# Kernel tuning notes

Measured on AMD Instinct MI355X. Metric: run time of the kernel, lower is better.

The kernel has to match this reference:

```python
import jax, jax.numpy as jnp
import numpy as np

EPS = 1e-5
MAX_NORM = 1.0 - 1e-5  # clamp for atanh / ball projection


def mob_add(u, v):
    # Mobius addition on each d_ball (last dim), c=1
    uv = jnp.sum(u * v, axis=-1, keepdims=True)
    uu = jnp.sum(u * u, axis=-1, keepdims=True)
    vv = jnp.sum(v * v, axis=-1, keepdims=True)
    num = (1.0 + 2.0 * uv + vv) * u + (1.0 - uu) * v
    den = 1.0 + 2.0 * uv + uu * vv
    return num / jnp.maximum(den, EPS)


def log_map_zero(y):
    # log map at origin, per ball (last dim)
    n = jnp.linalg.norm(y, axis=-1, keepdims=True)
    n_c = jnp.clip(n, EPS, MAX_NORM)
    return jnp.arctanh(n_c) * y / n_c


def mob_mat_mul_d(W, x, d):
    # W: (n_in, d, n_out, d); x: (B, n_in, d) -> (B, n_out, d)
    # Mobius matvec on the flattened product-ball representation.
    B = x.shape[0]
    x_f = x.reshape(B, -1)                      # (B, n_in*d)
    W_f = W.reshape(x_f.shape[-1], -1)          # (n_in*d, n_out*d)
    Mx = x_f @ W_f                              # (B, n_out*d)
    x_n = jnp.clip(jnp.linalg.norm(x_f, axis=-1, keepdims=True), EPS, MAX_NORM)
    Mx_n = jnp.maximum(jnp.linalg.norm(Mx, axis=-1, keepdims=True), EPS)
    res = jnp.tanh(Mx_n / x_n * jnp.arctanh(x_n)) * (Mx / Mx_n)
    return res.reshape(B, -1, d)


def mob_pointwise_prod(x, u):
    # diagonal Mobius scaling of hyperbolic x by euclidean gate u, per ball
    ux = u * x
    x_n = jnp.clip(jnp.linalg.norm(x, axis=-1, keepdims=True), EPS, MAX_NORM)
    ux_n = jnp.maximum(jnp.linalg.norm(ux, axis=-1, keepdims=True), EPS)
    return jnp.tanh(ux_n / x_n * jnp.arctanh(x_n)) * (ux / ux_n)


def transition(W, h, U, x, b, d):
    Wh = mob_mat_mul_d(W, h, d)
    Ux = mob_mat_mul_d(U, x, d)
    return mob_add(mob_add(Wh, Ux), b)


def setup_inputs() -> dict:
    key = jax.random.key(0)
    ks = jax.random.split(key, 8)
    B, I, H, D = 16384, 256, 256, 4
    k = (1.0 / H) ** 0.5
    # scale points to lie strictly inside the Poincare ball
    hyp_x = 0.02 * jax.random.normal(ks[0], (B, I, D), dtype=jnp.float32)
    hidden = 0.02 * jax.random.normal(ks[1], (B, H, D), dtype=jnp.float32)
    mk = lambda kk, n_in: jax.random.uniform(kk, (n_in, D, H, D), minval=-k, maxval=k, dtype=jnp.float32)
    return dict(
        hyp_x=hyp_x, hidden=hidden,
        w_z=mk(ks[2], H), w_r=mk(ks[3], H), w_h=mk(ks[4], H),
        u_z=mk(ks[5], I), u_r=mk(ks[6], I), u_h=mk(ks[7], I),
        b_z=jnp.zeros((H, D), jnp.float32),
        b_r=jnp.zeros((H, D), jnp.float32),
        b_h=jnp.zeros((H, D), jnp.float32),
    )


def reference(hyp_x, hidden, w_z, w_r, w_h, u_z, u_r, u_h, b_z, b_r, b_h):
    d = hyp_x.shape[-1]
    z = jax.nn.sigmoid(log_map_zero(transition(w_z, hidden, u_z, hyp_x, b_z, d)))
    r = jax.nn.sigmoid(log_map_zero(transition(w_r, hidden, u_r, hyp_x, b_r, d)))
    r_point_h = mob_pointwise_prod(hidden, r)
    # NOTE: original code uses u_r here (not u_h) -- kept faithful
    h_tilde = transition(w_h, r_point_h, u_r, hyp_x, b_h, d)
    minus_h_oplus_htilde = mob_add(-hidden, h_tilde)
    new_h = mob_add(hidden, mob_pointwise_prod(minus_h_oplus_htilde, z))
    return new_h
```

## Files before the change

kernel.cpp:

```cpp
#include <hip/hip_runtime.h>
#include <stdint.h>

#define EPSF 1e-5f
#define MAXNF (1.0f - 1e-5f)

typedef __attribute__((ext_vector_type(8))) short short8;
typedef __attribute__((ext_vector_type(4))) float floatx4;

__device__ __forceinline__ unsigned short f2bf(float f){
  union { float f; uint32_t u; } v; v.f = f;
  return (unsigned short)((v.u + 0x7FFFu + ((v.u >> 16) & 1u)) >> 16);
}
__device__ __forceinline__ float bf_lo(uint32_t u){
  union { uint32_t u; float f; } v; v.u = u << 16; return v.f;
}
__device__ __forceinline__ float bf_hi(uint32_t u){
  union { uint32_t u; float f; } v; v.u = u & 0xffff0000u; return v.f;
}
__device__ __forceinline__ uint32_t cvtpk(float lo, float hi){
  uint32_t r; asm("v_cvt_pk_bf16_f32 %0, %1, %2" : "=v"(r) : "v"(lo), "v"(hi));
  return r;
}
__device__ __forceinline__ float fsqrt(float x){ return __builtin_amdgcn_sqrtf(x); }

__device__ __forceinline__ float4 ld_ball(const unsigned short* rowp, int b){
  const uint2 u = *(const uint2*)(rowp + 4*b);
  return make_float4(bf_lo(u.x), bf_hi(u.x), bf_lo(u.y), bf_hi(u.y));
}
__device__ __forceinline__ void st_ball(unsigned short* rowp, int b, float4 f){
  uint2 u; u.x = cvtpk(f.x, f.y); u.y = cvtpk(f.z, f.w);
  *(uint2*)(rowp + 4*b) = u;
}

__device__ __forceinline__ void gload16(const void* g, void* l){
  __builtin_amdgcn_global_load_lds(
      (__attribute__((address_space(1))) void*)(uintptr_t)g,
      (__attribute__((address_space(3))) void*)l, 16, 0, 0);
}

__device__ __forceinline__ float fatanh(float x){
  return 0.5f * __logf(__fdividef(1.f + x, 1.f - x));
}
__device__ __forceinline__ float ftanh_pos(float x){
  const float t = __expf(-2.f * x);
  return __fdividef(1.f - t, 1.f + t);
}
__device__ __forceinline__ float fsig(float x){
  return __fdividef(1.f, 1.f + __expf(-x));
}

__device__ __forceinline__ float wsum(float v){
  #pragma unroll
  for (int o = 32; o; o >>= 1) v += __shfl_xor(v, o);
  return v;
}

__device__ __forceinline__ float dot4(const float4 a, const float4 b){
  return a.x*b.x + a.y*b.y + a.z*b.z + a.w*b.w;
}
__device__ __forceinline__ float4 scal4(const float4 a, float s){
  return make_float4(a.x*s, a.y*s, a.z*s, a.w*s);
}
__device__ __forceinline__ float clipn(float n){ return fminf(fmaxf(n, EPSF), MAXNF); }

__device__ __forceinline__ float4 mob_add4(const float4 u, const float4 v){
  const float uv = dot4(u,v), uu = dot4(u,u), vv = dot4(v,v);
  const float cu = 1.f + 2.f*uv + vv, cv = 1.f - uu;
  const float inv = __fdividef(1.f, fmaxf(1.f + 2.f*uv + uu*vv, EPSF));
  return make_float4((cu*u.x + cv*v.x)*inv, (cu*u.y + cv*v.y)*inv,
                     (cu*u.z + cv*v.z)*inv, (cu*u.w + cv*v.w)*inv);
}
__device__ __forceinline__ float4 logmap_sig4(const float4 y){
  const float nc = clipn(fsqrt(dot4(y,y)));
  const float s = __fdividef(fatanh(nc), nc);
  return make_float4(fsig(s*y.x), fsig(s*y.y), fsig(s*y.z), fsig(s*y.w));
}
__device__ __forceinline__ float4 mob_pp4(const float4 x, const float4 u){
  const float4 ux = make_float4(u.x*x.x, u.y*x.y, u.z*x.z, u.w*x.w);
  const float xn = clipn(fsqrt(dot4(x,x)));
  const float uxn = fmaxf(fsqrt(dot4(ux,ux)), EPSF);
  const float s = __fdividef(ftanh_pos(__fdividef(uxn, xn) * fatanh(xn)), uxn);
  return scal4(ux, s);
}

__global__ void cast_norm_k(const float* __restrict__ X, unsigned short* __restrict__ Xbf,
                            float* __restrict__ nrm){
  const int lane = threadIdx.x & 63;
  const int row  = blockIdx.x*4 + (threadIdx.x >> 6);
  const float4* xr = (const float4*)(X + (size_t)row*1024);
  unsigned short* br_ = Xbf + (size_t)row*1024;
  float ss = 0.f;
  #pragma unroll
  for (int i = 0; i < 4; ++i){
    const int b = lane + 64*i;
    const float4 v = xr[b];
    st_ball(br_, b, v);
    ss += dot4(v, v);
  }
  ss = wsum(ss);
  if (lane == 0) nrm[row] = fsqrt(ss);
}

__global__ void wcast_k(const float* __restrict__ W, unsigned short* __restrict__ Wt){
  __shared__ float tile[32][33];
  const int tx = threadIdx.x, ty = threadIdx.y;
  const int k0 = blockIdx.x * 32, n0 = blockIdx.y * 32;
  #pragma unroll
  for (int i = 0; i < 4; ++i)
    tile[ty + i*8][tx] = W[(size_t)(k0 + ty + i*8) * 1024 + n0 + tx];
  __syncthreads();
  #pragma unroll
  for (int i = 0; i < 4; ++i)
    Wt[(size_t)(n0 + ty + i*8) * 1024 + k0 + tx] = f2bf(tile[tx][ty + i*8]);
}

#define GBM 128
#define GBN 256
#define GBK 32
#define GKD 1024

__global__ __launch_bounds__(512) void gemm_k(const unsigned short* __restrict__ A,
                                              const unsigned short* __restrict__ Bt,
                                              unsigned short* __restrict__ C,
                                              int lda, int ldc, int lnx){
  __shared__ unsigned short smem[2*4096 + 2*8192];
  unsigned short* As = smem;
  unsigned short* Bs = smem + 2*4096;
  const int tid = threadIdx.x;
  const int lane = tid & 63, w = tid >> 6;
  const int wr = w >> 2, wc = w & 3;
  const int lr = lane & 15, kg = lane >> 4;
  const int wg  = blockIdx.x;
  const int xcd = wg & 7, q = wg >> 3;
  const int bx  = q & ((1 << lnx) - 1);
  const int by  = (xcd << 4) + (q >> lnx);
  const int row0 = by * GBM, col0 = bx * GBN;

  int aoff[4], boff[4];
  #pragma unroll
  for (int a = 0; a < 4; ++a){
    const int r = wr*64 + a*16 + lr;
    aoff[a] = r*32 + ((kg ^ ((r >> 1) & 3)) << 3);
  }
  #pragma unroll
  for (int b = 0; b < 4; ++b){
    const int r = wc*64 + b*16 + lr;
    boff[b] = r*32 + ((kg ^ ((r >> 1) & 3)) << 3);
  }

  floatx4 acc[4][4] = {};

  auto stage = [&](int buf, int kt){
    {
      const int flat = tid;
      const int r = flat >> 2, cp = flat & 3, c = cp ^ ((r >> 1) & 3);
      gload16(A + (size_t)(row0 + r)*lda + kt*GBK + c*8, As + buf*4096 + flat*8);
    }
    #pragma unroll
    for (int i = 0; i < 2; ++i){
      const int flat = i*512 + tid;
      const int r = flat >> 2, cp = flat & 3, c = cp ^ ((r >> 1) & 3);
      gload16(Bt + (size_t)(col0 + r)*GKD + kt*GBK + c*8, Bs + buf*8192 + flat*8);
    }
  };

  stage(0, 0);
  __syncthreads();
  int cur = 0;
  for (int kt = 0; kt < GKD/GBK; ++kt){
    if (kt + 1 < GKD/GBK) stage(cur ^ 1, kt + 1);
    const unsigned short* as = As + cur*4096;
    const unsigned short* bs = Bs + cur*8192;
    short8 af[4], bfv[4];
    #pragma unroll
    for (int a = 0; a < 4; ++a) af[a] = *(const short8*)(as + aoff[a]);
    #pragma unroll
    for (int b = 0; b < 4; ++b) bfv[b] = *(const short8*)(bs + boff[b]);
    #pragma unroll
    for (int a = 0; a < 4; ++a)
      #pragma unroll
      for (int b = 0; b < 4; ++b)
        acc[a][b] = __builtin_amdgcn_mfma_f32_16x16x32_bf16(af[a], bfv[b], acc[a][b], 0, 0, 0);
    __syncthreads();
    cur ^= 1;
  }

  const int crow0 = row0 + wr*64;
  const int ccol = col0 + wc*64 + lr;
  #pragma unroll
  for (int a = 0; a < 4; ++a){
    #pragma unroll
    for (int j = 0; j < 4; ++j){
      const int r = crow0 + a*16 + kg*4 + j;
      unsigned short* cp = C + (size_t)r*ldc + ccol;
      #pragma unroll
      for (int b = 0; b < 4; ++b) cp[b*16] = f2bf(acc[a][b][j]);
    }
  }
}

__global__ __launch_bounds__(256) __attribute__((amdgpu_waves_per_eu(4,4)))
void epi1_k(unsigned short* C1, unsigned short* C2, const unsigned short* hbf,
            const float* bz, const float* br,
            const float* h_nrm, const float* x_nrm, float* rph_nrm){
  const int lane = threadIdx.x & 63;
  const int row  = blockIdx.x*4 + (threadIdx.x >> 6);
  unsigned short* c1lo = C1 + (size_t)row*2048;
  unsigned short* c1hi = c1lo + 1024;
  unsigned short* c2lo = C2 + (size_t)row*2048;
  unsigned short* c2hi = c2lo + 1024;
  const unsigned short* hr = hbf + (size_t)row*1024;

  float4 mzh[4], mrh[4], mzx[4], mrx[4];
  float s0 = 0.f, s1 = 0.f, s2 = 0.f, s3 = 0.f;
  #pragma unroll
  for (int i = 0; i < 4; ++i){
    const int b = lane + 64*i;
    mzh[i] = ld_ball(c1lo, b); mrh[i] = ld_ball(c1hi, b);
    mzx[i] = ld_ball(c2lo, b); mrx[i] = ld_ball(c2hi, b);
    s0 += dot4(mzh[i], mzh[i]); s1 += dot4(mzx[i], mzx[i]);
    s2 += dot4(mrh[i], mrh[i]); s3 += dot4(mrx[i], mrx[i]);
  }
  s0 = wsum(s0); s1 = wsum(s1); s2 = wsum(s2); s3 = wsum(s3);

  const float nMzh = fmaxf(fsqrt(s0), EPSF);
  const float nMzx = fmaxf(fsqrt(s1), EPSF);
  const float nMrh = fmaxf(fsqrt(s2), EPSF);
  const float nMrx = fmaxf(fsqrt(s3), EPSF);
  const float hnc = clipn(h_nrm[row]), xnc = clipn(x_nrm[row]);
  const float atH = fatanh(hnc), atX = fatanh(xnc);
  const float swz = __fdividef(ftanh_pos(__fdividef(nMzh, hnc)*atH), nMzh);
  const float suz = __fdividef(ftanh_pos(__fdividef(nMzx, xnc)*atX), nMzx);
  const float swr = __fdividef(ftanh_pos(__fdividef(nMrh, hnc)*atH), nMrh);
  const float sur = __fdividef(ftanh_pos(__fdividef(nMrx, xnc)*atX), nMrx);

  float sr = 0.f;
  #pragma unroll
  for (int i = 0; i < 4; ++i){
    const int b = lane + 64*i;
    const float4 bz4 = ((const float4*)bz)[b];
    const float4 br4 = ((const float4*)br)[b];
    const float4 z4  = logmap_sig4(mob_add4(mob_add4(scal4(mzh[i],swz), scal4(mzx[i],suz)), bz4));
    const float4 UxR = scal4(mrx[i], sur);
    const float4 r4  = logmap_sig4(mob_add4(mob_add4(scal4(mrh[i],swr), UxR), br4));
    st_ball(c1lo, b, z4);
    st_ball(c1hi, b, UxR);
    const float4 h4  = ld_ball(hr, b);
    const float4 rph = mob_pp4(h4, r4);
    st_ball(c2lo, b, rph);
    sr += dot4(rph, rph);
  }
  sr = wsum(sr);
  if (lane == 0) rph_nrm[row] = fsqrt(sr);
}

__global__ __launch_bounds__(256) __attribute__((amdgpu_waves_per_eu(4,4)))
void epi2_k(const unsigned short* C1, const unsigned short* C2,
            const unsigned short* hbf, const float* bh,
            const float* rph_nrm, float* out){
  const int lane = threadIdx.x & 63;
  const int row  = blockIdx.x*4 + (threadIdx.x >> 6);
  const unsigned short* c1lo = C1 + (size_t)row*2048;
  const unsigned short* c1hi = c1lo + 1024;
  const unsigned short* c2hi = C2 + (size_t)row*2048 + 1024;
  const unsigned short* hr = hbf + (size_t)row*1024;
  float4* outr = (float4*)(out + (size_t)row*1024);

  float4 mh[4];
  float ss = 0.f;
  #pragma unroll
  for (int i = 0; i < 4; ++i){
    mh[i] = ld_ball(c2hi, lane + 64*i);
    ss += dot4(mh[i], mh[i]);
  }
  ss = wsum(ss);
  const float nMh = fmaxf(fsqrt(ss), EPSF);
  const float rnc = clipn(rph_nrm[row]);
  const float swh = __fdividef(ftanh_pos(__fdividef(nMh, rnc)*fatanh(rnc)), nMh);

  #pragma unroll
  for (int i = 0; i < 4; ++i){
    const int b = lane + 64*i;
    const float4 WhH = scal4(mh[i], swh);
    const float4 Ux4 = ld_ball(c1hi, b);
    const float4 bh4 = ((const float4*)bh)[b];
    const float4 ht  = mob_add4(mob_add4(WhH, Ux4), bh4);
    const float4 h4  = ld_ball(hr, b);
    const float4 nh4 = make_float4(-h4.x, -h4.y, -h4.z, -h4.w);
    const float4 m4  = mob_add4(nh4, ht);
    const float4 z4  = ld_ball(c1lo, b);
    const float4 p4  = mob_pp4(m4, z4);
    outr[b] = mob_add4(h4, p4);
  }
}

extern "C" void kernel_launch(void* const* d_in, const int* in_sizes, int n_in,
                              void* d_out, int out_size, void* d_ws, size_t ws_size,
                              hipStream_t stream) {
  (void)in_sizes; (void)n_in; (void)out_size; (void)ws_size;
  const float* hyp_x  = (const float*)d_in[0];
  const float* hidden = (const float*)d_in[1];
  const float* w_z = (const float*)d_in[2];
  const float* w_r = (const float*)d_in[3];
  const float* w_h = (const float*)d_in[4];
  const float* u_z = (const float*)d_in[5];
  const float* u_r = (const float*)d_in[6];
  const float* b_z = (const float*)d_in[8];
  const float* b_r = (const float*)d_in[9];
  const float* b_h = (const float*)d_in[10];
  float* out = (float*)d_out;

  const size_t NROW = 16384, MAT = NROW*1024;
  unsigned short* hbf = (unsigned short*)d_ws;
  unsigned short* xbf = hbf + MAT;
  unsigned short* C1  = xbf + MAT;
  unsigned short* wzr = C1 + 2*MAT;
  unsigned short* uzr = wzr + 2*1048576;
  unsigned short* wht = uzr + 2*1048576;
  float* h_n   = (float*)(wht + 1048576);
  float* x_n   = h_n + NROW;
  float* rph_n = x_n + NROW;
  unsigned short* C2 = (unsigned short*)d_out;

  cast_norm_k<<<dim3(4096), dim3(256), 0, stream>>>(hidden, hbf, h_n);
  cast_norm_k<<<dim3(4096), dim3(256), 0, stream>>>(hyp_x, xbf, x_n);

  dim3 wg(32, 32), wb(32, 8);
  wcast_k<<<wg, wb, 0, stream>>>(w_z, wzr);
  wcast_k<<<wg, wb, 0, stream>>>(w_r, wzr + 1048576);
  wcast_k<<<wg, wb, 0, stream>>>(u_z, uzr);
  wcast_k<<<wg, wb, 0, stream>>>(u_r, uzr + 1048576);
  wcast_k<<<wg, wb, 0, stream>>>(w_h, wht);

  gemm_k<<<dim3(1024), dim3(512), 0, stream>>>(hbf, wzr, C1, 1024, 2048, 3);
  gemm_k<<<dim3(1024), dim3(512), 0, stream>>>(xbf, uzr, C2, 1024, 2048, 3);

  epi1_k<<<dim3(4096), dim3(256), 0, stream>>>(C1, C2, hbf, b_z, b_r, h_n, x_n, rph_n);

  gemm_k<<<dim3(512), dim3(512), 0, stream>>>(C2, wht, C2 + 1024, 2048, 2048, 2);

  epi2_k<<<dim3(4096), dim3(256), 0, stream>>>(C1, C2, hbf, b_h, rph_n, out);
}
```

Measured before the change: 335.3 us.

## Replace GEMM with 256x256 tile, 8-wave ping-pong pipelined kernel

Swaps the 128x256, BK=32 double-buffered bf16 GEMM for a 256x256 tile with BK=64, 128KB of LDS and a fine-grained schedule. Loads for tiles t+1 and t+2 are interleaved between four MFMA quadrants, with explicit vmcnt waits, barriers and s_setprio. Each workgroup handles twice the output, so the grid halves. The aim is more data reuse per LDS byte and better overlap of global loads with MFMA, in exchange for higher register and LDS pressure and fewer workgroups, which may not fill all CUs.

```diff
diff --git a/kernel.cpp b/kernel.cpp
--- a/kernel.cpp
+++ b/kernel.cpp
@@ -114,87 +114,96 @@
     Wt[(size_t)(n0 + ty + i*8) * 1024 + k0 + tx] = f2bf(tile[tx][ty + i*8]);
 }
 
-#define GBM 128
-#define GBN 256
-#define GBK 32
-#define GKD 1024
-
-__global__ __launch_bounds__(512) void gemm_k(const unsigned short* __restrict__ A,
-                                              const unsigned short* __restrict__ Bt,
-                                              unsigned short* __restrict__ C,
-                                              int lda, int ldc, int lnx){
-  __shared__ unsigned short smem[2*4096 + 2*8192];
-  unsigned short* As = smem;
-  unsigned short* Bs = smem + 2*4096;
+#define NT 16
+
+#define BARFENCE do { __builtin_amdgcn_s_barrier(); asm volatile("" ::: "memory"); } while(0)
+#define LDA4(dst, MO) do { _Pragma("unroll") for (int m_=0;m_<4;++m_) \
+  _Pragma("unroll") for (int k_=0;k_<2;++k_) \
+    dst[m_][k_] = *(const short8*)(smem + bufb*32768 + abase + (MO+m_)*2048 + ((((k_<<2)+kg)^x7)<<4)); } while(0)
+#define LDB2(dst, NO) do { _Pragma("unroll") for (int n_=0;n_<2;++n_) \
+  _Pragma("unroll") for (int k_=0;k_<2;++k_) \
+    dst[n_][k_] = *(const short8*)(smem + bufb*32768 + bbase + (NO+n_)*2048 + ((((k_<<2)+kg)^x7)<<4)); } while(0)
+#define QUAD(AF, MO, BF, NO) do { _Pragma("unroll") for (int m_=0;m_<4;++m_) \
+  _Pragma("unroll") for (int n_=0;n_<2;++n_) \
+  _Pragma("unroll") for (int k_=0;k_<2;++k_) \
+    acc[MO+m_][NO+n_] = __builtin_amdgcn_mfma_f32_16x16x32_bf16(AF[m_][k_], BF[n_][k_], acc[MO+m_][NO+n_], 0,0,0); } while(0)
+
+__global__ __launch_bounds__(512, 2) void gemm8_k(const unsigned short* __restrict__ A,
+                                                  const unsigned short* __restrict__ Bt,
+                                                  unsigned short* __restrict__ C,
+                                                  int lda, int ldc, int lnx){
+  __shared__ unsigned char smem[131072];
   const int tid = threadIdx.x;
   const int lane = tid & 63, w = tid >> 6;
-  const int wr = w >> 2, wc = w & 3;
+  const int wm = w >> 2, wn = w & 3;
   const int lr = lane & 15, kg = lane >> 4;
+  const int x7 = lr & 7;
+
   const int wg  = blockIdx.x;
   const int xcd = wg & 7, q = wg >> 3;
   const int bx  = q & ((1 << lnx) - 1);
-  const int by  = (xcd << 4) + (q >> lnx);
-  const int row0 = by * GBM, col0 = bx * GBN;
-
-  int aoff[4], boff[4];
-  #pragma unroll
-  for (int a = 0; a < 4; ++a){
-    const int r = wr*64 + a*16 + lr;
-    aoff[a] = r*32 + ((kg ^ ((r >> 1) & 3)) << 3);
-  }
-  #pragma unroll
-  for (int b = 0; b < 4; ++b){
-    const int r = wc*64 + b*16 + lr;
-    boff[b] = r*32 + ((kg ^ ((r >> 1) & 3)) << 3);
-  }
-
-  floatx4 acc[4][4] = {};
-
-  auto stage = [&](int buf, int kt){
-    {
-      const int flat = tid;
-      const int r = flat >> 2, cp = flat & 3, c = cp ^ ((r >> 1) & 3);
-      gload16(A + (size_t)(row0 + r)*lda + kt*GBK + c*8, As + buf*4096 + flat*8);
-    }
+  const int by  = (xcd << 3) + (q >> lnx);
+  const int row0 = by * 256, col0 = bx * 256;
+
+  const int abase = (wm*128 + lr)*128;
+  const int bbase = 65536 + (wn*64 + lr)*128;
+
+  floatx4 acc[8][4] = {};
+
+  auto stageH = [&](int regionByte, const unsigned short* src, int srow0, int ld, int kt){
     #pragma unroll
-    for (int i = 0; i < 2; ++i){
-      const int flat = i*512 + tid;
-      const int r = flat >> 2, cp = flat & 3, c = cp ^ ((r >> 1) & 3);
-      gload16(Bt + (size_t)(col0 + r)*GKD + kt*GBK + c*8, Bs + buf*8192 + flat*8);
+    for (int call = 0; call < 2; ++call){
+      const int L  = (call << 9) + tid;
+      const int rl = L >> 3;
+      const int cc = (L & 7) ^ (rl & 7);
+      gload16(src + (size_t)(srow0 + rl)*ld + kt*64 + cc*8,
+              smem + regionByte + L*16);
     }
   };
-
-  stage(0, 0);
-  __syncthreads();
-  int cur = 0;
-  for (int kt = 0; kt < GKD/GBK; ++kt){
-    if (kt + 1 < GKD/GBK) stage(cur ^ 1, kt + 1);
-    const unsigned short* as = As + cur*4096;
-    const unsigned short* bs = Bs + cur*8192;
-    short8 af[4], bfv[4];
-    #pragma unroll
-    for (int a = 0; a < 4; ++a) af[a] = *(const short8*)(as + aoff[a]);
-    #pragma unroll
-    for (int b = 0; b < 4; ++b) bfv[b] = *(const short8*)(bs + boff[b]);
-    #pragma unroll
-    for (int a = 0; a < 4; ++a)
-      #pragma unroll
-      for (int b = 0; b < 4; ++b)
-        acc[a][b] = __builtin_amdgcn_mfma_f32_16x16x32_bf16(af[a], bfv[b], acc[a][b], 0, 0, 0);
-    __syncthreads();
-    cur ^= 1;
-  }
-
-  const int crow0 = row0 + wr*64;
-  const int ccol = col0 + wc*64 + lr;
-  #pragma unroll
-  for (int a = 0; a < 4; ++a){
+  auto stageA = [&](int kt, int h){ stageH((kt&1)*32768 + h*16384, A, row0 + h*128, lda, kt); };
+  auto stageB = [&](int kt, int h){ stageH(65536 + (kt&1)*32768 + h*16384, Bt, col0 + h*128, 1024, kt); };
+
+  stageA(0,0); stageA(0,1); stageB(0,0); stageB(0,1);
+  stageB(1,0); stageA(1,0); stageA(1,1);
+  asm volatile("s_waitcnt vmcnt(6)" ::: "memory");
+  __builtin_amdgcn_s_barrier();
+  asm volatile("" ::: "memory");
+
+  short8 aL[4][2], aH[4][2], bA[2][2], bB[2][2];
+
+  for (int t = 0; t < NT; ++t){
+    const int bufb = t & 1;
+    LDA4(aL, 0); LDB2(bA, 0);
+    if (t+1 < NT) stageB(t+1, 1);
+    BARFENCE;
+    __builtin_amdgcn_s_setprio(1); QUAD(aL, 0, bA, 0); __builtin_amdgcn_s_setprio(0);
+    BARFENCE;
+    LDB2(bB, 2);
+    BARFENCE;
+    __builtin_amdgcn_s_setprio(1); QUAD(aL, 0, bB, 2); __builtin_amdgcn_s_setprio(0);
+    BARFENCE;
+    LDA4(aH, 4);
+    if (t+2 < NT) stageB(t+2, 0);
+    BARFENCE;
+    __builtin_amdgcn_s_setprio(1); QUAD(aH, 4, bB, 2); __builtin_amdgcn_s_setprio(0);
+    BARFENCE;
+    if (t+2 < NT){ stageA(t+2, 0); stageA(t+2, 1); }
+    if (t+2 < NT)      asm volatile("s_waitcnt vmcnt(6)" ::: "memory");
+    else if (t+1 < NT) asm volatile("s_waitcnt vmcnt(0)" ::: "memory");
+    BARFENCE;
+    __builtin_amdgcn_s_setprio(1); QUAD(aH, 4, bA, 0); __builtin_amdgcn_s_setprio(0);
+    BARFENCE;
+  }
+
+  const int crow = row0 + wm*128;
+  const int ccol = col0 + wn*64 + lr;
+  #pragma unroll
+  for (int m = 0; m < 8; ++m){
     #pragma unroll
     for (int j = 0; j < 4; ++j){
-      const int r = crow0 + a*16 + kg*4 + j;
-      unsigned short* cp = C + (size_t)r*ldc + ccol;
+      unsigned short* cp = C + (size_t)(crow + m*16 + kg*4 + j)*ldc + ccol;
       #pragma unroll
-      for (int b = 0; b < 4; ++b) cp[b*16] = f2bf(acc[a][b][j]);
+      for (int n = 0; n < 4; ++n) cp[n*16] = f2bf(acc[m][n][j]);
     }
   }
 }
@@ -332,12 +341,12 @@
   wcast_k<<<wg, wb, 0, stream>>>(u_r, uzr + 1048576);
   wcast_k<<<wg, wb, 0, stream>>>(w_h, wht);
 
-  gemm_k<<<dim3(1024), dim3(512), 0, stream>>>(hbf, wzr, C1, 1024, 2048, 3);
-  gemm_k<<<dim3(1024), dim3(512), 0, stream>>>(xbf, uzr, C2, 1024, 2048, 3);
+  gemm8_k<<<dim3(512), dim3(512), 0, stream>>>(hbf, wzr, C1, 1024, 2048, 3);
+  gemm8_k<<<dim3(512), dim3(512), 0, stream>>>(xbf, uzr, C2, 1024, 2048, 3);
 
   epi1_k<<<dim3(4096), dim3(256), 0, stream>>>(C1, C2, hbf, b_z, b_r, h_n, x_n, rph_n);
 
-  gemm_k<<<dim3(512), dim3(512), 0, stream>>>(C2, wht, C2 + 1024, 2048, 2048, 2);
+  gemm8_k<<<dim3(256), dim3(512), 0, stream>>>(C2, wht, C2 + 1024, 2048, 2048, 2);
 
   epi2_k<<<dim3(4096), dim3(256), 0, stream>>>(C1, C2, hbf, b_h, rph_n, out);
 }
```

New measurement: 321.8 us. 1.04x faster.
